# Optimization experiments

Measured on AMD Instinct MI355X. Metric: run time of the kernel, lower is better.

Reference implementation:

```python
import jax, jax.numpy as jnp
import numpy as np


def setup_inputs() -> dict:
    key = jax.random.key(0)
    k = jax.random.split(key, 5)
    C, Cb = 128, 64
    x = jax.random.normal(k[0], (8, C, 64, 64), dtype=jnp.float32)
    s_in = 1.0 / np.sqrt(C)
    s_b = 1.0 / np.sqrt(Cb)
    w_theta = jax.random.normal(k[1], (Cb, C), dtype=jnp.float32) * s_in
    w_phi = jax.random.normal(k[2], (Cb, C), dtype=jnp.float32) * s_in
    w_g = jax.random.normal(k[3], (Cb, C), dtype=jnp.float32) * s_in
    w_last = jax.random.normal(k[4], (C, Cb), dtype=jnp.float32) * s_b
    return {"x": x, "w_theta": w_theta, "w_phi": w_phi, "w_g": w_g, "w_last": w_last}


def reference(x, w_theta, w_phi, w_g, w_last):
    B, C, H, W = x.shape
    xf = x.reshape(B, C, H * W)            # [B, C, N]
    theta = jnp.einsum('kc,bcn->bkn', w_theta, xf)   # [B, Cb, N]
    phi = jnp.einsum('kc,bcn->bkn', w_phi, xf)       # [B, Cb, N]
    g = jnp.einsum('kc,bcn->bkn', w_g, xf)           # [B, Cb, N]
    # attention over spatial positions: [B, N, N]
    attn = jax.nn.softmax(jnp.einsum('bkn,bkm->bnm', theta, phi), axis=-1)
    y = jnp.einsum('bnm,bkm->bkn', attn, g)          # [B, Cb, N]
    out = jnp.einsum('ck,bkn->bcn', w_last, y).reshape(B, C, H, W)
    return out + x
```

## Files before the change

### kernel.cpp

```cpp
#include <hip/hip_runtime.h>
#include <stdint.h>

typedef _Float16 h8v __attribute__((ext_vector_type(8)));
typedef _Float16 h4v __attribute__((ext_vector_type(4)));
typedef float f4v __attribute__((ext_vector_type(4)));
typedef _Float16 f16;

#define NB 8
#define CC 128
#define CB 64
#define NN 4096
#define L2E 1.4426950408889634f

#define GLD(gp, lp) __builtin_amdgcn_global_load_lds( \
    (const __attribute__((address_space(1))) void*)(gp), \
    (__attribute__((address_space(3))) void*)(lp), 16, 0, 0)

#define WAITV4() asm volatile("s_waitcnt vmcnt(4)" ::: "memory")
#define WAITV0() asm volatile("s_waitcnt vmcnt(0)" ::: "memory")
#define WAITL0() asm volatile("s_waitcnt lgkmcnt(0)" ::: "memory")

__global__ __launch_bounds__(256) void pack_w(
    const float* __restrict__ wth, const float* __restrict__ wph,
    const float* __restrict__ wg,  const float* __restrict__ wl,
    f16* __restrict__ wthp, f16* __restrict__ wphp,
    f16* __restrict__ wgp,  f16* __restrict__ wlp)
{
    const int t = blockIdx.x * 256 + threadIdx.x;
    for (int i = t; i < 8192; i += 2048){
        const int j = i & 7, lane = (i >> 3) & 63, kc = (i >> 9) & 3, ks = i >> 11;
        const int row = ks * 16 + (lane & 15);
        const int col = kc * 32 + ((lane >> 4) & 3) * 8 + j;
        wthp[i] = (f16)(wth[row * CC + col] * L2E);
        wphp[i] = (f16)(wph[row * CC + col]);
        wgp [i] = (f16)(wg [row * CC + col]);
    }
    for (int i = t; i < 8192; i += 2048){
        const int j = i & 7, lane = (i >> 3) & 63, kc = (i >> 9) & 1, cs = i >> 10;
        const int row = cs * 16 + (lane & 15);
        const int col = kc * 32 + ((lane >> 4) & 3) * 8 + j;
        wlp[i] = (f16)(wl[row * CB + col]);
    }
}

__global__ __launch_bounds__(256) void proj_kernel(
    const float* __restrict__ x, const f16* __restrict__ wthp,
    const f16* __restrict__ wphp, const f16* __restrict__ wgp,
    f16* __restrict__ thetaT, f16* __restrict__ phiT, f16* __restrict__ gbuf)
{
    __shared__ __align__(16) f16 xT[64][136];
    __shared__ __align__(16) f16 rep[4][16 * 72];
    const int b  = blockIdx.x & 7;
    const int n0 = (blockIdx.x >> 3) << 6;
    const int t  = threadIdx.x;

    #pragma unroll
    for (int i = 0; i < 8; i++){
        int v  = t + 256 * i;
        int c  = v >> 4;
        int j0 = (v & 15) << 2;
        const f4v xv = *(const f4v*)&x[((size_t)(b * CC + c)) * NN + n0 + j0];
        #pragma unroll
        for (int jj = 0; jj < 4; jj++) xT[j0 + jj][c] = (f16)xv[jj];
    }
    __syncthreads();

    const int w = t >> 6, lane = t & 63, quad = lane >> 4, l15 = lane & 15;
    const int rrow = lane >> 3, rcol = (lane & 7) * 8;

    h8v bx[4];
    #pragma unroll
    for (int kc = 0; kc < 4; kc++)
        bx[kc] = *(const h8v*)&xT[w * 16 + l15][kc * 32 + quad * 8];

    #pragma unroll
    for (int m3 = 0; m3 < 2; m3++){
        const f16* WP = (m3 == 0) ? wthp : wphp;
        f16* OUT      = (m3 == 0) ? thetaT : phiT;
        for (int ks = 0; ks < 4; ks++){
            f4v acc = {0.f, 0.f, 0.f, 0.f};
            #pragma unroll
            for (int kc = 0; kc < 4; kc++){
                const h8v af = *(const h8v*)&WP[(ks * 4 + kc) * 512 + lane * 8];
                acc = __builtin_amdgcn_mfma_f32_16x16x32_f16(af, bx[kc], acc, 0, 0, 0);
            }
            h4v pv;
            #pragma unroll
            for (int r = 0; r < 4; r++) pv[r] = (f16)acc[r];
            *(h4v*)&rep[w][l15 * 72 + ks * 16 + quad * 4] = pv;
        }
        #pragma unroll
        for (int j = 0; j < 2; j++){
            const h8v vv = *(const h8v*)&rep[w][(rrow + 8 * j) * 72 + rcol];
            *(h8v*)&OUT[((size_t)(b * NN + n0 + w * 16 + rrow + 8 * j)) * CB + rcol] = vv;
        }
    }

    h8v bw[4];
    #pragma unroll
    for (int kc = 0; kc < 4; kc++)
        bw[kc] = *(const h8v*)&wgp[(w * 4 + kc) * 512 + lane * 8];
    for (int ns = 0; ns < 4; ns++){
        f4v acc = {0.f, 0.f, 0.f, 0.f};
        #pragma unroll
        for (int kc = 0; kc < 4; kc++){
            const h8v af = *(const h8v*)&xT[ns * 16 + l15][kc * 32 + quad * 8];
            acc = __builtin_amdgcn_mfma_f32_16x16x32_f16(af, bw[kc], acc, 0, 0, 0);
        }
        h4v pv;
        #pragma unroll
        for (int r = 0; r < 4; r++) pv[r] = (f16)acc[r];
        *(h4v*)&rep[w][l15 * 72 + ns * 16 + quad * 4] = pv;
    }
    #pragma unroll
    for (int j = 0; j < 2; j++){
        const h8v vv = *(const h8v*)&rep[w][(rrow + 8 * j) * 72 + rcol];
        *(h8v*)&gbuf[((size_t)(b * CB + w * 16 + rrow + 8 * j)) * NN + n0 + rcol] = vv;
    }
}

union StageOrOut {
    struct { f16 ph[3][64 * 64]; f16 g[3][64 * 64]; } s;
    float fO[128][68];
};

__global__ __launch_bounds__(256, 2) void attn_kernel(
    const f16* __restrict__ thetaT, const f16* __restrict__ phiT,
    const f16* __restrict__ gbuf, const f16* __restrict__ wlp,
    const float* __restrict__ x, float* __restrict__ out)
{
    __shared__ __align__(16) StageOrOut sh;
    __shared__ __align__(16) f16 plds[4][16 * 72];

    const int b  = blockIdx.x & 7;
    const int q0 = (blockIdx.x >> 3) << 6;
    const int t  = threadIdx.x;
    const int w = t >> 6, lane = t & 63, quad = lane >> 4, l15 = lane & 15;
    const int n0 = q0 + w * 16;

    const size_t trow = ((size_t)(b * NN + n0 + l15)) * CB;
    const h8v a0 = *(const h8v*)&thetaT[trow + quad * 8];
    const h8v a1 = *(const h8v*)&thetaT[trow + 32 + quad * 8];

    const int srow = w * 16 + (lane >> 3);
    const int scb  = (lane & 7) ^ (lane >> 3);
    const f16* const pphB = phiT + ((size_t)(b * NN + srow)) * CB + scb * 8;
    const f16* const pggB = gbuf + ((size_t)(b * CB + srow)) * NN + scb * 8;

    const int so0 = (quad ^ (l15 & 7)) * 8;
    const int so1 = so0 ^ 32;

    auto STAGE = [&](int nb, int kb){
        const f16* s0 = pphB + (size_t)(kb * 64) * CB;
        const f16* s2 = pggB + kb * 64;
        f16* d0 = &sh.s.ph[nb][w * 1024];
        f16* d1 = &sh.s.g [nb][w * 1024];
        GLD(s0,            d0);
        GLD(s0 + 8 * CB,   d0 + 512);
        GLD(s2,            d1);
        GLD(s2 + 8 * NN,   d1 + 512);
    };

    STAGE(0, 0);
    STAGE(1, 1);

    float mrun = -1e30f, lrun = 0.f;
    const f4v zf = {0.f, 0.f, 0.f, 0.f};
    f4v o[4];
    #pragma unroll
    for (int tt = 0; tt < 4; tt++) o[tt] = zf;

    f16* const pw = &plds[w][0];

    int pb = 0;
    for (int kb = 0; kb < 64; kb++){
        if (kb < 63) WAITV4(); else WAITV0();
        WAITL0();
        __builtin_amdgcn_s_barrier();
        asm volatile("" ::: "memory");
        if (kb < 62) STAGE(pb == 0 ? 2 : pb - 1, kb + 2);

        f4v s[4];
        __builtin_amdgcn_s_setprio(1);
        #pragma unroll
        for (int tt = 0; tt < 4; tt++){
            const f16* pr = &sh.s.ph[pb][(tt * 16 + l15) * 64];
            const h8v pb0 = *(const h8v*)(pr + so0);
            const h8v pb1 = *(const h8v*)(pr + so1);
            f4v sv = zf;
            sv = __builtin_amdgcn_mfma_f32_16x16x32_f16(pb0, a0, sv, 0, 0, 0);
            sv = __builtin_amdgcn_mfma_f32_16x16x32_f16(pb1, a1, sv, 0, 0, 0);
            s[tt] = sv;
        }
        __builtin_amdgcn_s_setprio(0);

        float smax = fmaxf(fmaxf(s[0][0], s[0][1]), fmaxf(s[0][2], s[0][3]));
        #pragma unroll
        for (int tt = 1; tt < 4; tt++)
            smax = fmaxf(smax, fmaxf(fmaxf(s[tt][0], s[tt][1]), fmaxf(s[tt][2], s[tt][3])));
        smax = fmaxf(smax, __shfl_xor(smax, 16));
        smax = fmaxf(smax, __shfl_xor(smax, 32));

        if (__any(smax - mrun > 8.f)){
            const float mn = fmaxf(mrun, smax);
            const float alpha = __builtin_amdgcn_exp2f(mrun - mn);
            mrun = mn;
            lrun *= alpha;
            #pragma unroll
            for (int tt = 0; tt < 4; tt++)
                #pragma unroll
                for (int r = 0; r < 4; r++)
                    o[tt][r] *= alpha;
        }

        float lsum = 0.f;
        #pragma unroll
        for (int tt = 0; tt < 4; tt++){
            h4v pv;
            #pragma unroll
            for (int r = 0; r < 4; r++){
                float p = __builtin_amdgcn_exp2f(s[tt][r] - mrun);
                lsum += p;
                pv[r] = (f16)p;
            }
            *(h4v*)&pw[l15 * 72 + tt * 16 + quad * 4] = pv;
        }
        lrun += lsum;

        const h8v pa0 = *(const h8v*)&pw[l15 * 72 + quad * 8];
        const h8v pa1 = *(const h8v*)&pw[l15 * 72 + 32 + quad * 8];

        __builtin_amdgcn_s_setprio(1);
        #pragma unroll
        for (int tt = 0; tt < 4; tt++){
            const f16* gr = &sh.s.g[pb][(tt * 16 + l15) * 64];
            const h8v gb0 = *(const h8v*)(gr + so0);
            const h8v gb1 = *(const h8v*)(gr + so1);
            o[tt] = __builtin_amdgcn_mfma_f32_16x16x32_f16(gb0, pa0, o[tt], 0, 0, 0);
            o[tt] = __builtin_amdgcn_mfma_f32_16x16x32_f16(gb1, pa1, o[tt], 0, 0, 0);
        }
        __builtin_amdgcn_s_setprio(0);

        pb = (pb == 2) ? 0 : pb + 1;
    }

    lrun += __shfl_xor(lrun, 16);
    lrun += __shfl_xor(lrun, 32);
    const float inv = 1.0f / lrun;

    #pragma unroll
    for (int tt = 0; tt < 4; tt++){
        h4v yv;
        #pragma unroll
        for (int r = 0; r < 4; r++) yv[r] = (f16)(o[tt][r] * inv);
        *(h4v*)&pw[l15 * 72 + tt * 16 + quad * 4] = yv;
    }

    __syncthreads();

    const h8v yB0 = *(const h8v*)&pw[l15 * 72 + quad * 8];
    const h8v yB1 = *(const h8v*)&pw[l15 * 72 + 32 + quad * 8];
    #pragma unroll
    for (int cs = 0; cs < 8; cs++){
        const h8v wa0 = *(const h8v*)&wlp[(cs * 2 + 0) * 512 + lane * 8];
        const h8v wa1 = *(const h8v*)&wlp[(cs * 2 + 1) * 512 + lane * 8];
        f4v acc = zf;
        acc = __builtin_amdgcn_mfma_f32_16x16x32_f16(wa0, yB0, acc, 0, 0, 0);
        acc = __builtin_amdgcn_mfma_f32_16x16x32_f16(wa1, yB1, acc, 0, 0, 0);
        #pragma unroll
        for (int r = 0; r < 4; r++)
            sh.fO[cs * 16 + quad * 4 + r][w * 16 + l15] = acc[r];
    }
    __syncthreads();

    #pragma unroll
    for (int i = 0; i < 8; i++){
        const int row = i * 16 + (t >> 4);
        const int nf  = (t & 15) * 4;
        const f4v v = *(const f4v*)&sh.fO[row][nf];
        const size_t idx = ((size_t)(b * CC + row)) * NN + q0 + nf;
        const f4v xv = *(const f4v*)&x[idx];
        f4v ov;
        #pragma unroll
        for (int r = 0; r < 4; r++) ov[r] = v[r] + xv[r];
        *(f4v*)&out[idx] = ov;
    }
}

extern "C" void kernel_launch(void* const* d_in, const int* in_sizes, int n_in,
                              void* d_out, int out_size, void* d_ws, size_t ws_size,
                              hipStream_t stream)
{
    const float* x   = (const float*)d_in[0];
    const float* wth = (const float*)d_in[1];
    const float* wph = (const float*)d_in[2];
    const float* wg  = (const float*)d_in[3];
    const float* wl  = (const float*)d_in[4];
    float* out = (float*)d_out;

    f16* thetaT = (f16*)d_ws;
    f16* phiT   = thetaT + (size_t)NB * NN * CB;
    f16* gbuf   = phiT   + (size_t)NB * NN * CB;
    f16* wthp   = gbuf   + (size_t)NB * NN * CB;
    f16* wphp   = wthp + 8192;
    f16* wgp    = wphp + 8192;
    f16* wlp    = wgp  + 8192;

    pack_w<<<8, 256, 0, stream>>>(wth, wph, wg, wl, wthp, wphp, wgp, wlp);
    proj_kernel<<<NB * 64, 256, 0, stream>>>(x, wthp, wphp, wgp, thetaT, phiT, gbuf);
    attn_kernel<<<NB * 64, 256, 0, stream>>>(thetaT, phiT, gbuf, wlp, x, out);
}
```

Before: 156.5 us.

## Split attention key range across two wave groups with split-softmax merge

The attention kernel grows from 256 to 512 threads per block. Each 64-key tile is split into two 32-key halves, each handled by its own group of four waves, and the partial max, sum and output of the two groups are merged through LDS at the end. Staging is redistributed so that each wave issues two global-to-LDS loads per iteration, and the output projection is split between the two halves. The goal is more waves in flight to hide MFMA and softmax latency, at the cost of extra merge synchronisation, LDS traffic and a 512-thread occupancy requirement.

```diff
diff --git a/kernel.cpp b/kernel.cpp
--- a/kernel.cpp
+++ b/kernel.cpp
@@ -16,7 +16,7 @@
     (const __attribute__((address_space(1))) void*)(gp), \
     (__attribute__((address_space(3))) void*)(lp), 16, 0, 0)
 
-#define WAITV4() asm volatile("s_waitcnt vmcnt(4)" ::: "memory")
+#define WAITV2() asm volatile("s_waitcnt vmcnt(2)" ::: "memory")
 #define WAITV0() asm volatile("s_waitcnt vmcnt(0)" ::: "memory")
 #define WAITL0() asm volatile("s_waitcnt lgkmcnt(0)" ::: "memory")
 
@@ -119,50 +119,66 @@
     }
 }
 
-union StageOrOut {
-    struct { f16 ph[3][64 * 64]; f16 g[3][64 * 64]; } s;
-    float fO[128][68];
-};
-
-__global__ __launch_bounds__(256, 2) void attn_kernel(
+__global__ __launch_bounds__(512, 4) void attn_kernel(
     const f16* __restrict__ thetaT, const f16* __restrict__ phiT,
     const f16* __restrict__ gbuf, const f16* __restrict__ wlp,
     const float* __restrict__ x, float* __restrict__ out)
 {
-    __shared__ __align__(16) StageOrOut sh;
-    __shared__ __align__(16) f16 plds[4][16 * 72];
+    __shared__ __align__(16) char SM[59392];
+    f16*   const PH  = (f16*)SM;
+    f16*   const GG  = (f16*)(SM + 24576);
+    f16*   const PLD = (f16*)(SM + 49152);
+    float* const MG  = (float*)SM;
+    float* const ML  = (float*)(SM + 17408);
+    float* const FO  = (float*)SM;
+    f16*   const YY  = (f16*)(SM + 36864);
 
     const int b  = blockIdx.x & 7;
     const int q0 = (blockIdx.x >> 3) << 6;
     const int t  = threadIdx.x;
-    const int w = t >> 6, lane = t & 63, quad = lane >> 4, l15 = lane & 15;
-    const int n0 = q0 + w * 16;
+    const int w  = t >> 6;
+    const int lane = t & 63, quad = lane >> 4, l15 = lane & 15;
+    const int wq = w & 3;
+    const int h  = w >> 2;
+    const int n0 = q0 + wq * 16;
 
     const size_t trow = ((size_t)(b * NN + n0 + l15)) * CB;
     const h8v a0 = *(const h8v*)&thetaT[trow + quad * 8];
     const h8v a1 = *(const h8v*)&thetaT[trow + 32 + quad * 8];
 
-    const int srow = w * 16 + (lane >> 3);
-    const int scb  = (lane & 7) ^ (lane >> 3);
-    const f16* const pphB = phiT + ((size_t)(b * NN + srow)) * CB + scb * 8;
-    const f16* const pggB = gbuf + ((size_t)(b * CB + srow)) * NN + scb * 8;
+    const int seg  = w * 2;
+    const int tsel = seg >> 3;
+    const int kind = (seg >> 2) & 1;
+    const int qa   = seg & 3;
+    const f16* sA;  const f16* sB;  size_t adv;
+    if (kind == 0){
+        const int row = qa * 8 + (lane >> 3);
+        const int gr  = (lane & 7) ^ (lane >> 3);
+        sA = phiT + ((size_t)(b * NN + tsel * 32 + row)) * CB + gr * 8;
+        sB = sA + (size_t)8 * CB;
+        adv = (size_t)64 * CB;
+    } else {
+        const int row = qa * 16 + (lane >> 2);
+        const int gr  = (lane & 3) ^ ((lane >> 2) & 3);
+        sA = gbuf + ((size_t)(b * CB + row)) * NN + tsel * 32 + gr * 8;
+        sB = sA + (size_t)16 * NN;
+        adv = 64;
+    }
+    f16* const dBase = (kind == 0) ? PH : GG;
+    const int dOff = qa * 512;
 
     const int so0 = (quad ^ (l15 & 7)) * 8;
     const int so1 = so0 ^ 32;
-
-    auto STAGE = [&](int nb, int kb){
-        const f16* s0 = pphB + (size_t)(kb * 64) * CB;
-        const f16* s2 = pggB + kb * 64;
-        f16* d0 = &sh.s.ph[nb][w * 1024];
-        f16* d1 = &sh.s.g [nb][w * 1024];
-        GLD(s0,            d0);
-        GLD(s0 + 8 * CB,   d0 + 512);
-        GLD(s2,            d1);
-        GLD(s2 + 8 * NN,   d1 + 512);
-    };
-
-    STAGE(0, 0);
-    STAGE(1, 1);
+    const int go  = (quad ^ (l15 & 3)) * 8;
+
+    {
+        f16* d0 = dBase + (0 + tsel) * 2048 + dOff;
+        GLD(sA, d0);  GLD(sB, d0 + 512);
+        f16* d1 = dBase + (2 + tsel) * 2048 + dOff;
+        GLD(sA + adv, d1);  GLD(sB + adv, d1 + 512);
+    }
+    const f16* pA = sA + 2 * adv;
+    const f16* pB = sB + 2 * adv;
 
     float mrun = -1e30f, lrun = 0.f;
     const f4v zf = {0.f, 0.f, 0.f, 0.f};
@@ -170,21 +186,29 @@
     #pragma unroll
     for (int tt = 0; tt < 4; tt++) o[tt] = zf;
 
-    f16* const pw = &plds[w][0];
-
-    int pb = 0;
-    for (int kb = 0; kb < 64; kb++){
-        if (kb < 63) WAITV4(); else WAITV0();
+    f16* const PW = PLD + w * 640;
+
+    int rc = 0;
+    int rs = 2;
+    for (int m = 0; m < 64; m++){
+        if (m < 63) WAITV2(); else WAITV0();
         WAITL0();
         __builtin_amdgcn_s_barrier();
         asm volatile("" ::: "memory");
-        if (kb < 62) STAGE(pb == 0 ? 2 : pb - 1, kb + 2);
-
-        f4v s[4];
+        if (m < 62){
+            f16* d = dBase + (2 * rs + tsel) * 2048 + dOff;
+            GLD(pA, d);  GLD(pB, d + 512);
+            pA += adv;   pB += adv;
+        }
+        const int ct = 2 * rc + h;
+        const f16* phc = PH + ct * 2048;
+        const f16* ggc = GG + ct * 2048;
+
+        f4v s[2];
         __builtin_amdgcn_s_setprio(1);
         #pragma unroll
-        for (int tt = 0; tt < 4; tt++){
-            const f16* pr = &sh.s.ph[pb][(tt * 16 + l15) * 64];
+        for (int tt = 0; tt < 2; tt++){
+            const f16* pr = phc + (tt * 16 + l15) * 64;
             const h8v pb0 = *(const h8v*)(pr + so0);
             const h8v pb1 = *(const h8v*)(pr + so1);
             f4v sv = zf;
@@ -195,9 +219,7 @@
         __builtin_amdgcn_s_setprio(0);
 
         float smax = fmaxf(fmaxf(s[0][0], s[0][1]), fmaxf(s[0][2], s[0][3]));
-        #pragma unroll
-        for (int tt = 1; tt < 4; tt++)
-            smax = fmaxf(smax, fmaxf(fmaxf(s[tt][0], s[tt][1]), fmaxf(s[tt][2], s[tt][3])));
+        smax = fmaxf(smax, fmaxf(fmaxf(s[1][0], s[1][1]), fmaxf(s[1][2], s[1][3])));
         smax = fmaxf(smax, __shfl_xor(smax, 16));
         smax = fmaxf(smax, __shfl_xor(smax, 32));
 
@@ -215,7 +237,7 @@
 
         float lsum = 0.f;
         #pragma unroll
-        for (int tt = 0; tt < 4; tt++){
+        for (int tt = 0; tt < 2; tt++){
             h4v pv;
             #pragma unroll
             for (int r = 0; r < 4; r++){
@@ -223,45 +245,64 @@
                 lsum += p;
                 pv[r] = (f16)p;
             }
-            *(h4v*)&pw[l15 * 72 + tt * 16 + quad * 4] = pv;
+            *(h4v*)&PW[l15 * 40 + tt * 16 + quad * 4] = pv;
         }
         lrun += lsum;
 
-        const h8v pa0 = *(const h8v*)&pw[l15 * 72 + quad * 8];
-        const h8v pa1 = *(const h8v*)&pw[l15 * 72 + 32 + quad * 8];
+        const h8v pa = *(const h8v*)&PW[l15 * 40 + quad * 8];
 
         __builtin_amdgcn_s_setprio(1);
         #pragma unroll
-        for (int tt = 0; tt < 4; tt++){
-            const f16* gr = &sh.s.g[pb][(tt * 16 + l15) * 64];
-            const h8v gb0 = *(const h8v*)(gr + so0);
-            const h8v gb1 = *(const h8v*)(gr + so1);
-            o[tt] = __builtin_amdgcn_mfma_f32_16x16x32_f16(gb0, pa0, o[tt], 0, 0, 0);
-            o[tt] = __builtin_amdgcn_mfma_f32_16x16x32_f16(gb1, pa1, o[tt], 0, 0, 0);
+        for (int tt2 = 0; tt2 < 4; tt2++){
+            const h8v gb = *(const h8v*)(ggc + (tt2 * 16 + l15) * 32 + go);
+            o[tt2] = __builtin_amdgcn_mfma_f32_16x16x32_f16(gb, pa, o[tt2], 0, 0, 0);
         }
         __builtin_amdgcn_s_setprio(0);
 
-        pb = (pb == 2) ? 0 : pb + 1;
+        rc = (rc == 2) ? 0 : rc + 1;
+        rs = (rs == 2) ? 0 : rs + 1;
     }
 
     lrun += __shfl_xor(lrun, 16);
     lrun += __shfl_xor(lrun, 32);
-    const float inv = 1.0f / lrun;
-
-    #pragma unroll
-    for (int tt = 0; tt < 4; tt++){
-        h4v yv;
-        #pragma unroll
-        for (int r = 0; r < 4; r++) yv[r] = (f16)(o[tt][r] * inv);
-        *(h4v*)&pw[l15 * 72 + tt * 16 + quad * 4] = yv;
-    }
-
-    __syncthreads();
-
-    const h8v yB0 = *(const h8v*)&pw[l15 * 72 + quad * 8];
-    const h8v yB1 = *(const h8v*)&pw[l15 * 72 + 32 + quad * 8];
-    #pragma unroll
-    for (int cs = 0; cs < 8; cs++){
+
+    __syncthreads();
+
+    if (h == 1){
+        #pragma unroll
+        for (int tt2 = 0; tt2 < 4; tt2++)
+            *(f4v*)&MG[wq * 1088 + l15 * 68 + tt2 * 16 + quad * 4] = o[tt2];
+        if (lane < 16){
+            ML[wq * 32 + lane * 2 + 0] = mrun;
+            ML[wq * 32 + lane * 2 + 1] = lrun;
+        }
+    }
+    __syncthreads();
+
+    if (h == 0){
+        const float m4 = ML[wq * 32 + l15 * 2 + 0];
+        const float l4 = ML[wq * 32 + l15 * 2 + 1];
+        const float M  = fmaxf(mrun, m4);
+        const float e0 = __builtin_amdgcn_exp2f(mrun - M);
+        const float e1 = __builtin_amdgcn_exp2f(m4 - M);
+        const float inv = 1.0f / (lrun * e0 + l4 * e1);
+        #pragma unroll
+        for (int tt2 = 0; tt2 < 4; tt2++){
+            const f4v o4 = *(const f4v*)&MG[wq * 1088 + l15 * 68 + tt2 * 16 + quad * 4];
+            h4v yv;
+            #pragma unroll
+            for (int r = 0; r < 4; r++)
+                yv[r] = (f16)((o[tt2][r] * e0 + o4[r] * e1) * inv);
+            *(h4v*)&YY[(wq * 16 + l15) * 72 + tt2 * 16 + quad * 4] = yv;
+        }
+    }
+    __syncthreads();
+
+    const h8v yB0 = *(const h8v*)&YY[(wq * 16 + l15) * 72 + quad * 8];
+    const h8v yB1 = *(const h8v*)&YY[(wq * 16 + l15) * 72 + 32 + quad * 8];
+    #pragma unroll
+    for (int ci = 0; ci < 4; ci++){
+        const int cs = h * 4 + ci;
         const h8v wa0 = *(const h8v*)&wlp[(cs * 2 + 0) * 512 + lane * 8];
         const h8v wa1 = *(const h8v*)&wlp[(cs * 2 + 1) * 512 + lane * 8];
         f4v acc = zf;
@@ -269,15 +310,15 @@
         acc = __builtin_amdgcn_mfma_f32_16x16x32_f16(wa1, yB1, acc, 0, 0, 0);
         #pragma unroll
         for (int r = 0; r < 4; r++)
-            sh.fO[cs * 16 + quad * 4 + r][w * 16 + l15] = acc[r];
-    }
-    __syncthreads();
-
-    #pragma unroll
-    for (int i = 0; i < 8; i++){
-        const int row = i * 16 + (t >> 4);
+            FO[(cs * 16 + quad * 4 + r) * 68 + wq * 16 + l15] = acc[r];
+    }
+    __syncthreads();
+
+    #pragma unroll
+    for (int i = 0; i < 4; i++){
+        const int row = i * 32 + (t >> 4);
         const int nf  = (t & 15) * 4;
-        const f4v v = *(const f4v*)&sh.fO[row][nf];
+        const f4v v = *(const f4v*)&FO[row * 68 + nf];
         const size_t idx = ((size_t)(b * CC + row)) * NN + q0 + nf;
         const f4v xv = *(const f4v*)&x[idx];
         f4v ov;
@@ -308,5 +349,5 @@
 
     pack_w<<<8, 256, 0, stream>>>(wth, wph, wg, wl, wthp, wphp, wgp, wlp);
     proj_kernel<<<NB * 64, 256, 0, stream>>>(x, wthp, wphp, wgp, thetaT, phiT, gbuf);
-    attn_kernel<<<NB * 64, 256, 0, stream>>>(thetaT, phiT, gbuf, wlp, x, out);
+    attn_kernel<<<NB * 64, 512, 0, stream>>>(thetaT, phiT, gbuf, wlp, x, out);
 }
```

Measured after the change: 150.7 us. 3.7% less time.
